# Kernel tuning notes

Measured on AMD Instinct MI355X. Metric: run time of the kernel, lower is better.

The kernel has to match this reference:

```python
import jax, jax.numpy as jnp
import numpy as np
import math

B, T, E, H, R = 4, 1024, 1024, 16, 16
DH = E // H


def setup_inputs() -> dict:
    key = jax.random.key(0)
    ks = jax.random.split(key, 14)
    s = 0.02
    inp = {
        "X": jax.random.normal(ks[0], (B, T, E), dtype=jnp.float32),
        "mask": jnp.ones((B, T), dtype=jnp.float32),
        # full-rank frozen projections (torch Linear: y = x @ W.T + b)
        "Wq": jax.random.normal(ks[1], (E, E), dtype=jnp.float32) * s,
        "bq": jnp.zeros((E,), dtype=jnp.float32),
        "Wk": jax.random.normal(ks[2], (E, E), dtype=jnp.float32) * s,
        "bk": jnp.zeros((E,), dtype=jnp.float32),
        "Wv": jax.random.normal(ks[3], (E, E), dtype=jnp.float32) * s,
        "bv": jnp.zeros((E,), dtype=jnp.float32),
        # LoRA: A: [R, E], B: [E, R], no bias
        "Aq": jax.random.normal(ks[4], (R, E), dtype=jnp.float32) * s,
        "Bq": jax.random.normal(ks[5], (E, R), dtype=jnp.float32) * s,
        "Ak": jax.random.normal(ks[6], (R, E), dtype=jnp.float32) * s,
        "Bk": jax.random.normal(ks[7], (E, R), dtype=jnp.float32) * s,
        "Av": jax.random.normal(ks[8], (R, E), dtype=jnp.float32) * s,
        "Bv": jax.random.normal(ks[9], (E, R), dtype=jnp.float32) * s,
    }
    return inp


def _split_heads(x):
    # [B, T, E] -> [B, H, T, Dh]
    b, t, _ = x.shape
    return x.reshape(b, t, H, DH).transpose(0, 2, 1, 3)


def reference(X, mask, Wq, bq, Wk, bk, Wv, bv, Aq, Bq, Ak, Bk, Av, Bv):
    def proj(W, b, A, Bl):
        # frozen linear + LoRA: X @ W.T + b + (X @ A.T) @ B.T
        return X @ W.T + b + (X @ A.T) @ Bl.T

    q = _split_heads(proj(Wq, bq, Aq, Bq))  # [B,H,T,Dh]
    k = _split_heads(proj(Wk, bk, Ak, Bk))
    v = _split_heads(proj(Wv, bv, Av, Bv))

    t = q.shape[2]
    scores = jnp.einsum("bhid,bhjd->bhij", q, k) / math.sqrt(E)
    # causal: positions with col > row set to -inf (triu offset=1)
    causal = jnp.triu(jnp.ones((t, t), dtype=bool), k=1)
    scores = jnp.where(causal, -jnp.inf, scores)
    # NOTE: faithful to source: softmax over axis=dims-2 (query/row axis)
    attn = jax.nn.softmax(scores, axis=2)
    # post-softmax padding-mask multiply, broadcast [B,1,1,T]
    attn = attn * mask[:, None, None, :]
    out = jnp.einsum("bhij,bhjd->bhid", attn, v)  # [B,H,T,Dh]
    return out.transpose(0, 2, 1, 3).reshape(X.shape[0], t, E)
```

## Files before the change

kernel.cpp:

```cpp
#include <hip/hip_runtime.h>
#include <stdint.h>

typedef __bf16 v8bf __attribute__((ext_vector_type(8)));
typedef float  v4f  __attribute__((ext_vector_type(4)));

__device__ __forceinline__ uint16_t f2bf(float f){
  union { float f; uint32_t u; } v; v.f = f;
  uint32_t r = v.u + 0x7FFFu + ((v.u >> 16) & 1u);
  return (uint16_t)(r >> 16);
}
__device__ __forceinline__ float bf2f(uint16_t u){
  union { uint32_t u; float f; } v; v.u = ((uint32_t)u) << 16; return v.f;
}
__device__ __forceinline__ v4f vzero(){ v4f z = {0.f,0.f,0.f,0.f}; return z; }

__device__ __forceinline__ void gld16(const uint16_t* __restrict__ g, uint16_t* l){
  __builtin_amdgcn_global_load_lds((const __attribute__((address_space(1))) void*)g,
                                   (__attribute__((address_space(3))) void*)l, 16, 0, 0);
}

__device__ __forceinline__ void ld64(uint4 r[2], const uint16_t* __restrict__ g, int ldg, int tid){
  int row = tid >> 2, c = (tid & 3) * 16;
  r[0] = *(const uint4*)(g + (size_t)row * ldg + c);
  r[1] = *(const uint4*)(g + (size_t)row * ldg + c + 8);
}
__device__ __forceinline__ void st64(uint16_t* __restrict__ s, const uint4 r[2], int tid){
  int row = tid >> 2, c = (tid & 3) * 16;
  *(uint4*)(s + row * 72 + c) = r[0];
  *(uint4*)(s + row * 72 + c + 8) = r[1];
}
__device__ __forceinline__ void stage64(uint16_t* s, const uint16_t* g, int ldg, int tid){
  uint4 r[2]; ld64(r, g, ldg, tid); st64(s, r, tid);
}

__global__ void k_prep(const float* __restrict__ X, uint16_t* __restrict__ Xb,
                       float* __restrict__ csum,
                       const float* __restrict__ Wq, const float* __restrict__ Aq, const float* __restrict__ Bq,
                       const float* __restrict__ Wk, const float* __restrict__ Ak, const float* __restrict__ Bk,
                       const float* __restrict__ Wv, const float* __restrict__ Av, const float* __restrict__ Bv,
                       uint16_t* __restrict__ Wo){
  int bid = blockIdx.x, tid = threadIdx.x;
  if (bid < 2048){
    int i = (bid * 256 + tid) * 8;
    float4 a = *(const float4*)(X + i);
    float4 b = *(const float4*)(X + i + 4);
    union { uint16_t h[8]; uint4 v; } o;
    o.h[0]=f2bf(a.x); o.h[1]=f2bf(a.y); o.h[2]=f2bf(a.z); o.h[3]=f2bf(a.w);
    o.h[4]=f2bf(b.x); o.h[5]=f2bf(b.y); o.h[6]=f2bf(b.z); o.h[7]=f2bf(b.w);
    *(uint4*)(Xb + i) = o.v;
    if (bid < 64)
      ((float4*)csum)[bid * 256 + tid] = make_float4(0.f, 0.f, 0.f, 0.f);
  } else {
    int w = bid - 2048;
    int y = w >> 12;
    const float* W  = (y == 0) ? Wq : (y == 1) ? Wk : Wv;
    const float* A  = (y == 0) ? Aq : (y == 1) ? Ak : Av;
    const float* Bm = (y == 0) ? Bq : (y == 1) ? Bk : Bv;
    int idx = (w & 4095) * 256 + tid;
    int f = idx >> 10, k = idx & 1023;
    float acc = W[idx];
    #pragma unroll
    for (int r = 0; r < 16; ++r) acc += Bm[f * 16 + r] * A[r * 1024 + k];
    Wo[(size_t)y * 1048576 + idx] = f2bf(acc);
  }
}

__global__ __launch_bounds__(256, 4)
void k_gemm(const uint16_t* __restrict__ Ag, const uint16_t* __restrict__ Bg,
            const float* __restrict__ qb, const float* __restrict__ kb,
            const float* __restrict__ vb, uint16_t* __restrict__ Cg){
  __shared__ __align__(16) uint16_t smem[16896];
  uint16_t* As = smem;
  uint16_t* Bs = smem + 8192;
  int tid = threadIdx.x, lane = tid & 63, wid = tid >> 6;
  int l15 = lane & 15, lg = lane >> 4;
  int wr = wid >> 1, wc = wid & 1;
  int bid = blockIdx.x, xcd = bid & 7, idx = bid >> 3;
  int nb = xcd * 96 + idx;
  int mt = nb / 24, nt = nb - mt * 24;
  int m0 = mt * 128, n0 = nt * 128;

  int lr  = lane >> 3;
  int lcs = (((lane & 7) ^ lr)) * 8;
  const uint16_t* Abase = Ag + (size_t)(m0 + wid * 32 + lr) * 1024 + lcs;
  const uint16_t* Bbase = Bg + (size_t)(n0 + wid * 32 + lr) * 1024 + lcs;
  uint16_t* Alds = As + wid * 32 * 64;
  uint16_t* Blds = Bs + wid * 32 * 64;

  int sw = l15 & 7;

  v4f acc[4][4];
  #pragma unroll
  for (int a = 0; a < 4; ++a)
    #pragma unroll
    for (int c = 0; c < 4; ++c) acc[a][c] = vzero();

  for (int kk = 0; kk < 1024; kk += 64){
    __syncthreads();
    #pragma unroll
    for (int i = 0; i < 4; ++i){
      gld16(Abase + (size_t)(i * 8) * 1024 + kk, Alds + i * 8 * 64);
      gld16(Bbase + (size_t)(i * 8) * 1024 + kk, Blds + i * 8 * 64);
    }
    __syncthreads();
    #pragma unroll
    for (int kc = 0; kc < 2; ++kc){
      v8bf af[4], bfr[4];
      int cs = ((kc * 4 + lg) ^ sw) * 8;
      #pragma unroll
      for (int mi = 0; mi < 4; ++mi)
        af[mi] = *(const v8bf*)(As + (wr * 64 + mi * 16 + l15) * 64 + cs);
      #pragma unroll
      for (int nj = 0; nj < 4; ++nj)
        bfr[nj] = *(const v8bf*)(Bs + (wc * 64 + nj * 16 + l15) * 64 + cs);
      #pragma unroll
      for (int mi = 0; mi < 4; ++mi)
        #pragma unroll
        for (int nj = 0; nj < 4; ++nj)
          acc[mi][nj] = __builtin_amdgcn_mfma_f32_16x16x32_bf16(af[mi], bfr[nj], acc[mi][nj], 0, 0, 0);
    }
  }
  __syncthreads();
  uint16_t* Ct = smem;
  #pragma unroll
  for (int nj = 0; nj < 4; ++nj){
    int n = n0 + wc * 64 + nj * 16 + l15;
    float bv_ = (n < 1024) ? qb[n] : (n < 2048) ? kb[n - 1024] : vb[n - 2048];
    #pragma unroll
    for (int mi = 0; mi < 4; ++mi)
      #pragma unroll
      for (int r = 0; r < 4; ++r){
        int ml = wr * 64 + mi * 16 + lg * 4 + r;
        Ct[ml * 132 + wc * 64 + nj * 16 + l15] = f2bf(acc[mi][nj][r] + bv_);
      }
  }
  __syncthreads();
  {
    int row = tid >> 1;
    int c0  = (tid & 1) * 64;
    uint16_t* gp = Cg + (size_t)(m0 + row) * 3072 + n0 + c0;
    const uint16_t* sp = Ct + row * 132 + c0;
    #pragma unroll
    for (int c = 0; c < 8; ++c)
      *(uint4*)(gp + c * 8) = *(const uint4*)(sp + c * 8);
  }
}

__global__ __launch_bounds__(256, 4)
void k_score(const uint16_t* __restrict__ QKVg, float* __restrict__ csum,
             uint16_t* __restrict__ Pws){
  __shared__ __align__(16) uint16_t Ka[4096], Kb2[4096], Qs[4096], PsA[4096], PsB[4096];
  int tid = threadIdx.x, lane = tid & 63, wid = tid >> 6;
  int l15 = lane & 15, lg = lane >> 4;
  int wr = wid >> 1, wc = wid & 1;
  int sw = l15 & 7;
  int bid = blockIdx.x, xcd = bid & 7, idx = bid >> 3;
  int bh = xcd * 8 + (idx & 7);
  int rest = idx >> 3;
  int pr = rest & 7, ph = rest >> 3;
  int b = bh >> 4, h = bh & 15;
  int jtA = pr, jtB = 15 - pr;
  const uint16_t* Qb = QKVg + (size_t)b * 1024 * 3072 + h * 64;
  const uint16_t* Kb = QKVg + (size_t)b * 1024 * 3072 + 1024 + h * 64;
  uint16_t* Pbh = Pws + (size_t)bh * 557056;

  int lr  = lane >> 3;
  int lcs = ((lane & 7) ^ lr) * 8;
  {
    const uint16_t* sA = Kb + (size_t)(jtA * 64 + wid * 16 + lr) * 3072 + lcs;
    const uint16_t* sB = Kb + (size_t)(jtB * 64 + wid * 16 + lr) * 3072 + lcs;
    gld16(sA, Ka + wid * 16 * 64);
    gld16(sA + (size_t)8 * 3072, Ka + (wid * 16 + 8) * 64);
    gld16(sB, Kb2 + wid * 16 * 64);
    gld16(sB + (size_t)8 * 3072, Kb2 + (wid * 16 + 8) * 64);
  }
  int it0 = jtA + ph;
  v4f cpA[2] = {vzero(), vzero()}, cpB[2] = {vzero(), vzero()};
  for (int it = it0; it < 16; it += 2){
    __syncthreads();
    {
      const uint16_t* sQ = Qb + (size_t)(it * 64 + wid * 16 + lr) * 3072 + lcs;
      gld16(sQ, Qs + wid * 16 * 64);
      gld16(sQ + (size_t)8 * 3072, Qs + (wid * 16 + 8) * 64);
    }
    __syncthreads();
    bool doB = (it >= jtB);
    v4f sa[2][2], sb[2][2];
    #pragma unroll
    for (int a = 0; a < 2; ++a)
      #pragma unroll
      for (int c = 0; c < 2; ++c){ sa[a][c] = vzero(); sb[a][c] = vzero(); }
    #pragma unroll
    for (int kc = 0; kc < 2; ++kc){
      int cs = ((kc * 4 + lg) ^ sw) * 8;
      v8bf aq[2], k1[2], k2[2];
      #pragma unroll
      for (int ni = 0; ni < 2; ++ni)
        aq[ni] = *(const v8bf*)(Qs + (wc * 32 + ni * 16 + l15) * 64 + cs);
      #pragma unroll
      for (int mj = 0; mj < 2; ++mj)
        k1[mj] = *(const v8bf*)(Ka + (wr * 32 + mj * 16 + l15) * 64 + cs);
      __builtin_amdgcn_s_setprio(1);
      #pragma unroll
      for (int mj = 0; mj < 2; ++mj)
        #pragma unroll
        for (int ni = 0; ni < 2; ++ni)
          sa[mj][ni] = __builtin_amdgcn_mfma_f32_16x16x32_bf16(k1[mj], aq[ni], sa[mj][ni], 0, 0, 0);
      __builtin_amdgcn_s_setprio(0);
      if (doB){
        #pragma unroll
        for (int mj = 0; mj < 2; ++mj)
          k2[mj] = *(const v8bf*)(Kb2 + (wr * 32 + mj * 16 + l15) * 64 + cs);
        __builtin_amdgcn_s_setprio(1);
        #pragma unroll
        for (int mj = 0; mj < 2; ++mj)
          #pragma unroll
          for (int ni = 0; ni < 2; ++ni)
            sb[mj][ni] = __builtin_amdgcn_mfma_f32_16x16x32_bf16(k2[mj], aq[ni], sb[mj][ni], 0, 0, 0);
        __builtin_amdgcn_s_setprio(0);
      }
    }
    bool diagA = (it == jtA), diagB = (it == jtB);
    #pragma unroll
    for (int mj = 0; mj < 2; ++mj)
      #pragma unroll
      for (int ni = 0; ni < 2; ++ni){
        int iL = wc * 32 + ni * 16 + l15;
        int jb = wr * 32 + mj * 16 + lg * 4;
        int off = iL * 64 + (((jb >> 3) ^ (iL & 7)) * 8) + (jb & 7);
        {
          float e0 = (!diagA || jb + 0 <= iL) ? __expf(sa[mj][ni][0] * 0.03125f) : 0.f;
          float e1 = (!diagA || jb + 1 <= iL) ? __expf(sa[mj][ni][1] * 0.03125f) : 0.f;
          float e2 = (!diagA || jb + 2 <= iL) ? __expf(sa[mj][ni][2] * 0.03125f) : 0.f;
          float e3 = (!diagA || jb + 3 <= iL) ? __expf(sa[mj][ni][3] * 0.03125f) : 0.f;
          v4f e4 = {e0, e1, e2, e3};
          cpA[mj] += e4;
          uint2 pk;
          pk.x = (uint32_t)f2bf(e0) | ((uint32_t)f2bf(e1) << 16);
          pk.y = (uint32_t)f2bf(e2) | ((uint32_t)f2bf(e3) << 16);
          *(uint2*)(PsA + off) = pk;
        }
        if (doB){
          float e0 = (!diagB || jb + 0 <= iL) ? __expf(sb[mj][ni][0] * 0.03125f) : 0.f;
          float e1 = (!diagB || jb + 1 <= iL) ? __expf(sb[mj][ni][1] * 0.03125f) : 0.f;
          float e2 = (!diagB || jb + 2 <= iL) ? __expf(sb[mj][ni][2] * 0.03125f) : 0.f;
          float e3 = (!diagB || jb + 3 <= iL) ? __expf(sb[mj][ni][3] * 0.03125f) : 0.f;
          v4f e4 = {e0, e1, e2, e3};
          cpB[mj] += e4;
          uint2 pk;
          pk.x = (uint32_t)f2bf(e0) | ((uint32_t)f2bf(e1) << 16);
          pk.y = (uint32_t)f2bf(e2) | ((uint32_t)f2bf(e3) << 16);
          *(uint2*)(PsB + off) = pk;
        }
      }
    __syncthreads();
    {
      int tri = it * (it + 1) / 2;
      uint16_t* dA = Pbh + (size_t)(tri + jtA) * 4096 + tid * 16;
      uint4 a0 = *(const uint4*)(PsA + tid * 16);
      uint4 a1 = *(const uint4*)(PsA + tid * 16 + 8);
      *(uint4*)dA = a0; *(uint4*)(dA + 8) = a1;
      if (doB){
        uint16_t* dB = Pbh + (size_t)(tri + jtB) * 4096 + tid * 16;
        uint4 b0 = *(const uint4*)(PsB + tid * 16);
        uint4 b1 = *(const uint4*)(PsB + tid * 16 + 8);
        *(uint4*)dB = b0; *(uint4*)(dB + 8) = b1;
      }
    }
  }
  #pragma unroll
  for (int mj = 0; mj < 2; ++mj)
    #pragma unroll
    for (int m = 1; m <= 8; m <<= 1)
      #pragma unroll
      for (int r = 0; r < 4; ++r){
        cpA[mj][r] += __shfl_xor(cpA[mj][r], m, 64);
        cpB[mj][r] += __shfl_xor(cpB[mj][r], m, 64);
      }
  if (l15 == 0){
    #pragma unroll
    for (int mj = 0; mj < 2; ++mj)
      #pragma unroll
      for (int r = 0; r < 4; ++r){
        int jo = wr * 32 + mj * 16 + lg * 4 + r;
        atomicAdd(&csum[(size_t)bh * 1024 + jtA * 64 + jo], cpA[mj][r]);
        atomicAdd(&csum[(size_t)bh * 1024 + jtB * 64 + jo], cpB[mj][r]);
      }
  }
}

__global__ __launch_bounds__(256)
void k_vprep(const uint16_t* __restrict__ QKVg, const float* __restrict__ csum,
             const float* __restrict__ mask, uint16_t* __restrict__ Vp){
  __shared__ __align__(16) uint16_t Vs[128 * 72];
  __shared__ float scb[128];
  int tid = threadIdx.x;
  int bid = blockIdx.x, xcd = bid & 7, idx = bid >> 3;
  int bh = xcd * 8 + (idx & 7);
  int jt = idx >> 3;
  int b = bh >> 4, h = bh & 15;
  int j0 = jt * 128;
  stage64(Vs,           QKVg + ((size_t)(b * 1024 + j0)) * 3072 + 2048 + h * 64, 3072, tid);
  stage64(Vs + 64 * 72, QKVg + ((size_t)(b * 1024 + j0 + 64)) * 3072 + 2048 + h * 64, 3072, tid);
  if (tid < 128) scb[tid] = mask[b * 1024 + j0 + tid] / csum[(size_t)bh * 1024 + j0 + tid];
  __syncthreads();
  int d = tid >> 2, jc = (tid & 3) * 32;
  #pragma unroll
  for (int g8 = 0; g8 < 4; ++g8){
    union { uint16_t h[8]; uint4 v; } o;
    #pragma unroll
    for (int e = 0; e < 8; ++e){
      int j = jc + g8 * 8 + e;
      o.h[e] = f2bf(bf2f(Vs[j * 72 + d]) * scb[j]);
    }
    int jl = jc + g8 * 8;
    int wbase = jl & ~63;
    int c = (jl & 63) >> 3;
    int jphys = wbase + ((c ^ (d & 7)) * 8);
    *(uint4*)(Vp + (size_t)bh * 65536 + (size_t)d * 1024 + j0 + jphys) = o.v;
  }
}

__global__ __launch_bounds__(256, 4)
void k_pv(const uint16_t* __restrict__ Pws, const uint16_t* __restrict__ Vp,
          float* __restrict__ out){
  __shared__ __align__(16) uint16_t smem[16384];
  int tid = threadIdx.x, lane = tid & 63, l15 = lane & 15, lg = lane >> 4, wid = tid >> 6;
  int sw = l15 & 7;
  int bid = blockIdx.x, xcd = bid & 7, idx = bid >> 3;
  int bh = xcd * 8 + (idx & 7);
  int it = idx >> 3;
  int b = bh >> 4, h = bh & 15;
  const uint16_t* Pbh = Pws + (size_t)bh * 557056 + (size_t)(it * (it + 1) / 2) * 4096;
  const uint16_t* Vb  = Vp + (size_t)bh * 65536;
  v4f oacc[4];
  #pragma unroll
  for (int c = 0; c < 4; ++c) oacc[c] = vzero();

  #define PV_STAGE(buf, jt) do {                                                        \
    uint16_t* Pt_ = smem + (buf) * 8192;                                                \
    uint16_t* Vt_ = Pt_ + 4096;                                                         \
    const uint16_t* ps = Pbh + (size_t)(jt) * 4096;                                     \
    gld16(ps + wid * 512 + lane * 8,        Pt_ + wid * 512);                           \
    gld16(ps + 2048 + wid * 512 + lane * 8, Pt_ + 2048 + wid * 512);                    \
    const uint16_t* vs = Vb + (size_t)(jt) * 64;                                        \
    gld16(vs + (size_t)(wid * 8 + (lane >> 3)) * 1024 + (lane & 7) * 8,      Vt_ + wid * 512); \
    gld16(vs + (size_t)(32 + wid * 8 + (lane >> 3)) * 1024 + (lane & 7) * 8, Vt_ + 2048 + wid * 512); \
  } while (0)

  PV_STAGE(0, 0);
  __syncthreads();
  int cur = 0;
  for (int jt = 0; jt <= it; ++jt){
    if (jt < it) PV_STAGE(cur ^ 1, jt + 1);
    const uint16_t* Pt = smem + cur * 8192;
    const uint16_t* Vt = Pt + 4096;
    #pragma unroll
    for (int kc = 0; kc < 2; ++kc){
      int cs = ((kc * 4 + lg) ^ sw) * 8;
      v8bf pa = *(const v8bf*)(Pt + (wid * 16 + l15) * 64 + cs);
      v8bf vb_[4];
      #pragma unroll
      for (int dj = 0; dj < 4; ++dj)
        vb_[dj] = *(const v8bf*)(Vt + (dj * 16 + l15) * 64 + cs);
      __builtin_amdgcn_s_setprio(1);
      #pragma unroll
      for (int dj = 0; dj < 4; ++dj)
        oacc[dj] = __builtin_amdgcn_mfma_f32_16x16x32_bf16(pa, vb_[dj], oacc[dj], 0, 0, 0);
      __builtin_amdgcn_s_setprio(0);
    }
    __syncthreads();
    cur ^= 1;
  }
  #undef PV_STAGE
  float* Of = (float*)smem;
  #pragma unroll
  for (int dj = 0; dj < 4; ++dj)
    #pragma unroll
    for (int r = 0; r < 4; ++r)
      Of[(wid * 16 + lg * 4 + r) * 68 + dj * 16 + l15] = oacc[dj][r];
  __syncthreads();
  {
    int row = tid >> 2, c0 = (tid & 3) * 16;
    float* gp = out + ((size_t)(b * 1024) + it * 64 + row) * 1024 + h * 64 + c0;
    const float* sp = Of + row * 68 + c0;
    #pragma unroll
    for (int c = 0; c < 4; ++c)
      *(float4*)(gp + c * 4) = *(const float4*)(sp + c * 4);
  }
}

extern "C" void kernel_launch(void* const* d_in, const int* in_sizes, int n_in,
                              void* d_out, int out_size, void* d_ws, size_t ws_size,
                              hipStream_t stream) {
  (void)in_sizes; (void)n_in; (void)out_size; (void)ws_size;
  const float* X    = (const float*)d_in[0];
  const float* mask = (const float*)d_in[1];
  const float* Wq   = (const float*)d_in[2];
  const float* bq   = (const float*)d_in[3];
  const float* Wk   = (const float*)d_in[4];
  const float* bk   = (const float*)d_in[5];
  const float* Wv   = (const float*)d_in[6];
  const float* bv   = (const float*)d_in[7];
  const float* Aq   = (const float*)d_in[8];
  const float* Bq   = (const float*)d_in[9];
  const float* Ak   = (const float*)d_in[10];
  const float* Bk   = (const float*)d_in[11];
  const float* Av   = (const float*)d_in[12];
  const float* Bv   = (const float*)d_in[13];
  float* out = (float*)d_out;

  uint16_t* Xb   = (uint16_t*)d_ws;
  uint16_t* Weff = Xb + (size_t)4096 * 1024;
  uint16_t* QKV  = Weff + (size_t)3 * 1024 * 1024;
  uint16_t* Vp   = QKV + (size_t)4096 * 3072;
  float*    csum = (float*)(Vp + (size_t)64 * 64 * 1024);
  uint16_t* Pws  = (uint16_t*)((char*)d_ws + 48496640ULL);

  k_prep<<<14336, 256, 0, stream>>>(X, Xb, csum, Wq, Aq, Bq, Wk, Ak, Bk, Wv, Av, Bv, Weff);
  k_gemm<<<768, 256, 0, stream>>>(Xb, Weff, bq, bk, bv, QKV);
  k_score<<<1024, 256, 0, stream>>>(QKV, csum, Pws);
  k_vprep<<<512, 256, 0, stream>>>(QKV, csum, mask, Vp);
  k_pv<<<1024, 256, 0, stream>>>(Pws, Vp, out);
}
```

Before: 100.9 us.

## Double-buffer Q tiles and write P directly to global in k_score

Q tiles for k_score are now double-buffered in shared memory, with the next tile's async load issued before the current tile is computed. This removes one barrier per iteration and hides load latency. The P tiles are also written straight to global memory as 8-byte uint2 stores instead of being staged in shared memory and copied out with 16-byte stores. That frees shared memory and removes a pass, at the cost of narrower, more scattered global writes.

New measurement: 99.71 us. Within noise of the previous version (-1.2%).

```diff
diff --git a/kernel.cpp b/kernel.cpp
--- a/kernel.cpp
+++ b/kernel.cpp
@@ -149,7 +149,7 @@
 __global__ __launch_bounds__(256, 4)
 void k_score(const uint16_t* __restrict__ QKVg, float* __restrict__ csum,
              uint16_t* __restrict__ Pws){
-  __shared__ __align__(16) uint16_t Ka[4096], Kb2[4096], Qs[4096], PsA[4096], PsB[4096];
+  __shared__ __align__(16) uint16_t Ka[4096], Kb2[4096], Qs2[8192];
   int tid = threadIdx.x, lane = tid & 63, wid = tid >> 6;
   int l15 = lane & 15, lg = lane >> 4;
   int wr = wid >> 1, wc = wid & 1;
@@ -175,15 +175,22 @@
     gld16(sB + (size_t)8 * 3072, Kb2 + (wid * 16 + 8) * 64);
   }
   int it0 = jtA + ph;
+  {
+    const uint16_t* sQ = Qb + (size_t)(it0 * 64 + wid * 16 + lr) * 3072 + lcs;
+    gld16(sQ, Qs2 + wid * 16 * 64);
+    gld16(sQ + (size_t)8 * 3072, Qs2 + (wid * 16 + 8) * 64);
+  }
+  __syncthreads();
+  int cur = 0;
   v4f cpA[2] = {vzero(), vzero()}, cpB[2] = {vzero(), vzero()};
   for (int it = it0; it < 16; it += 2){
-    __syncthreads();
-    {
-      const uint16_t* sQ = Qb + (size_t)(it * 64 + wid * 16 + lr) * 3072 + lcs;
-      gld16(sQ, Qs + wid * 16 * 64);
-      gld16(sQ + (size_t)8 * 3072, Qs + (wid * 16 + 8) * 64);
-    }
-    __syncthreads();
+    if (it + 2 < 16){
+      uint16_t* qd = Qs2 + (cur ^ 1) * 4096;
+      const uint16_t* sQ = Qb + (size_t)((it + 2) * 64 + wid * 16 + lr) * 3072 + lcs;
+      gld16(sQ, qd + wid * 16 * 64);
+      gld16(sQ + (size_t)8 * 3072, qd + (wid * 16 + 8) * 64);
+    }
+    const uint16_t* Qcur = Qs2 + cur * 4096;
     bool doB = (it >= jtB);
     v4f sa[2][2], sb[2][2];
     #pragma unroll
@@ -196,7 +203,7 @@
       v8bf aq[2], k1[2], k2[2];
       #pragma unroll
       for (int ni = 0; ni < 2; ++ni)
-        aq[ni] = *(const v8bf*)(Qs + (wc * 32 + ni * 16 + l15) * 64 + cs);
+        aq[ni] = *(const v8bf*)(Qcur + (wc * 32 + ni * 16 + l15) * 64 + cs);
       #pragma unroll
       for (int mj = 0; mj < 2; ++mj)
         k1[mj] = *(const v8bf*)(Ka + (wr * 32 + mj * 16 + l15) * 64 + cs);
@@ -221,6 +228,9 @@
       }
     }
     bool diagA = (it == jtA), diagB = (it == jtB);
+    int tri = it * (it + 1) / 2;
+    uint16_t* dA = Pbh + (size_t)(tri + jtA) * 4096;
+    uint16_t* dB = Pbh + (size_t)(tri + jtB) * 4096;
     #pragma unroll
     for (int mj = 0; mj < 2; ++mj)
       #pragma unroll
@@ -238,7 +248,7 @@
           uint2 pk;
           pk.x = (uint32_t)f2bf(e0) | ((uint32_t)f2bf(e1) << 16);
           pk.y = (uint32_t)f2bf(e2) | ((uint32_t)f2bf(e3) << 16);
-          *(uint2*)(PsA + off) = pk;
+          *(uint2*)(dA + off) = pk;
         }
         if (doB){
           float e0 = (!diagB || jb + 0 <= iL) ? __expf(sb[mj][ni][0] * 0.03125f) : 0.f;
@@ -250,23 +260,11 @@
           uint2 pk;
           pk.x = (uint32_t)f2bf(e0) | ((uint32_t)f2bf(e1) << 16);
           pk.y = (uint32_t)f2bf(e2) | ((uint32_t)f2bf(e3) << 16);
-          *(uint2*)(PsB + off) = pk;
+          *(uint2*)(dB + off) = pk;
         }
       }
     __syncthreads();
-    {
-      int tri = it * (it + 1) / 2;
-      uint16_t* dA = Pbh + (size_t)(tri + jtA) * 4096 + tid * 16;
-      uint4 a0 = *(const uint4*)(PsA + tid * 16);
-      uint4 a1 = *(const uint4*)(PsA + tid * 16 + 8);
-      *(uint4*)dA = a0; *(uint4*)(dA + 8) = a1;
-      if (doB){
-        uint16_t* dB = Pbh + (size_t)(tri + jtB) * 4096 + tid * 16;
-        uint4 b0 = *(const uint4*)(PsB + tid * 16);
-        uint4 b1 = *(const uint4*)(PsB + tid * 16 + 8);
-        *(uint4*)dB = b0; *(uint4*)(dB + 8) = b1;
-      }
-    }
+    cur ^= 1;
   }
   #pragma unroll
   for (int mj = 0; mj < 2; ++mj)
```
